# Kernel optimization log

Measured on AMD Instinct MI355X. Metric: run time of the kernel, lower is better.

The kernel has to match this reference:

```python
import jax, jax.numpy as jnp
import numpy as np

TEMP1, TEMP2, TEMP3 = 4.0, 5.0, 10.0
NORM_EPS = 1e-12   # F.normalize eps
COS_EPS = 1e-8     # custom_cosine_similarity eps


def setup_inputs() -> dict:
    key = jax.random.key(0)
    k1, k2 = jax.random.split(key)
    vis_embeds = jax.random.normal(k1, (16, 16, 16, 16, 128), dtype=jnp.float32)
    txt_embeds = jax.random.normal(k2, (16, 64, 128), dtype=jnp.float32)
    return {"vis_embeds": vis_embeds, "txt_embeds": txt_embeds}


def reference(vis_embeds, txt_embeds):
    # vis_embeds: [bs, h, w, d, E]; txt_embeds: [bs, T, E] (uniform token_len)
    bs, h, w, d, E = vis_embeds.shape
    S = h * w * d
    # L2-normalize along embedding dim (F.normalize)
    vn = vis_embeds / jnp.clip(jnp.linalg.norm(vis_embeds, axis=-1, keepdims=True), NORM_EPS)
    vn = vn.reshape(bs, S, E)                      # context, flattened source
    tn = txt_embeds / jnp.clip(jnp.linalg.norm(txt_embeds, axis=-1, keepdims=True), NORM_EPS)
    # attention_fn, vectorized over the outer loop index i (txt sample):
    # attn0[i,b,s,t] = <context_b[s], query_i[t]>
    attn0 = jnp.einsum('bse,ite->ibst', vn, tn)    # [bs_txt, bs_vis, S, T]
    s1 = jax.nn.softmax(attn0, axis=-1)            # softmax over query tokens t
    a = jax.nn.softmax(TEMP1 * jnp.swapaxes(s1, -1, -2), axis=-1)  # [i,b,t,s], softmax over s
    # weighted context: [i,b,t,E]
    wc = jnp.einsum('ibts,bse->ibte', a, vn)
    # custom cosine similarity along E between txt tokens and weighted context
    num = jnp.einsum('ibte,ite->ibt', wc, tn)
    w1 = jnp.linalg.norm(tn, axis=-1)              # [i,t] (== 1 up to normalize eps)
    w2 = jnp.linalg.norm(wc, axis=-1)              # [i,b,t]
    cos = num / jnp.clip(w1[:, None, :] * w2, COS_EPS)
    # row_sim: mul temp2, exp, sum over tokens (agg='sum'), log
    row = jnp.log(jnp.sum(jnp.exp(TEMP2 * cos), axis=-1))  # [i_txt, b_vis]
    sims = row.T * TEMP3                           # [b_vis, i_txt] matches torch cat(dim=1)
    labels = jnp.arange(bs)
    logp0 = jax.nn.log_softmax(sims, axis=-1)
    logp1 = jax.nn.log_softmax(sims.T, axis=-1)
    loss0 = -jnp.mean(logp0[labels, labels])
    loss1 = -jnp.mean(logp1[labels, labels])
    loss = (loss0 + loss1) / 2.0
    # att_maps: for sample i the original keeps attn[i] -> diagonal of [i,b,...]
    att_maps = a[labels, labels].reshape(bs, -1, h, w, d)  # [bs, T, h, w, d]
    return loss, att_maps
```

## Files before the change

kernel.cpp:

```cpp
#include <hip/hip_runtime.h>

constexpr int BS = 16;
constexpr int S  = 4096;
constexpr int E  = 128;
constexpr int T  = 64;
constexpr int NSP = 4;
constexpr int SSEG = S / NSP;
constexpr int CH = 128;
constexpr int NCH = SSEG / CH;
constexpr int ETS = 136;
constexpr int TNS = 136;
constexpr int PTS = 264;

constexpr long VN_OFF  = 0;
constexpr long VNT_OFF = (long)BS * S * E;
constexpr long WS_P    = (long)BS * S * E;
constexpr long WS_SIMS = WS_P + (long)256 * NSP * 8192;

typedef __attribute__((ext_vector_type(8))) short bf16x8;
typedef __attribute__((ext_vector_type(4))) float f32x4;

__device__ __forceinline__ unsigned short f2bf(float x) {
    unsigned u = __float_as_uint(x);
    u += 0x7FFFu + ((u >> 16) & 1u);
    return (unsigned short)(u >> 16);
}
__device__ __forceinline__ float bf2f(unsigned short v) {
    return __uint_as_float(((unsigned)v) << 16);
}

__global__ __launch_bounds__(512, 2)
void prep_kernel(const float* __restrict__ vis, unsigned short* __restrict__ wsv)
{
    __shared__ unsigned short Lt[128 * PTS];
    const int tid  = threadIdx.x;
    const int b    = blockIdx.x >> 5;
    const int tile = blockIdx.x & 31;
    const int s0   = tile * 128;
    const float* visb = vis + ((long)b * S + s0) * E;
    unsigned short* vn  = wsv + VN_OFF  + ((long)b * S + s0) * E;
    unsigned short* vnT = wsv + VNT_OFF + (long)b * E * S;

    {
        const int pp = tid >> 3, ee = tid & 7;
        const float* rA = visb + (long)(pp << 1) * E + (ee << 1);
        float2 va[8], vb[8];
        float sa = 0.f, sb = 0.f;
#pragma unroll
        for (int k = 0; k < 8; ++k) {
            va[k] = *(const float2*)(rA + (k << 4));
            vb[k] = *(const float2*)(rA + E + (k << 4));
            sa = fmaf(va[k].x, va[k].x, fmaf(va[k].y, va[k].y, sa));
            sb = fmaf(vb[k].x, vb[k].x, fmaf(vb[k].y, vb[k].y, sb));
        }
        sa += __shfl_xor(sa, 1); sa += __shfl_xor(sa, 2); sa += __shfl_xor(sa, 4);
        sb += __shfl_xor(sb, 1); sb += __shfl_xor(sb, 2); sb += __shfl_xor(sb, 4);
        const float ia = 1.0f / fmaxf(sqrtf(sa), 1e-12f);
        const float ib = 1.0f / fmaxf(sqrtf(sb), 1e-12f);
        const long r0 = (long)(pp << 1) * E, r1 = r0 + E;
#pragma unroll
        for (int k = 0; k < 8; ++k) {
            const int e0 = (ee << 1) + (k << 4);
            const unsigned ax = f2bf(va[k].x * ia), ay = f2bf(va[k].y * ia);
            const unsigned bx = f2bf(vb[k].x * ib), by = f2bf(vb[k].y * ib);
            *(unsigned*)&Lt[e0 * PTS + (pp << 1)]       = ax | (bx << 16);
            *(unsigned*)&Lt[(e0 + 1) * PTS + (pp << 1)] = ay | (by << 16);
            *(unsigned*)&vn[r0 + e0] = ax | (ay << 16);
            *(unsigned*)&vn[r1 + e0] = bx | (by << 16);
        }
    }
    __syncthreads();
    {
        const int e = tid >> 2, sseg = (tid & 3) << 5;
#pragma unroll
        for (int k = 0; k < 4; ++k) {
            const bf16x8 v = *(const bf16x8*)&Lt[e * PTS + sseg + (k << 3)];
            *(bf16x8*)&vnT[(long)e * S + s0 + sseg + (k << 3)] = v;
        }
    }
}

__global__ __launch_bounds__(512, 4)
void clip_main_kernel(const unsigned short* __restrict__ wsv,
                      const float* __restrict__ txt,
                      float* __restrict__ d_out,
                      float* __restrict__ wsf)
{
    __shared__ unsigned short ET[T * ETS];
    __shared__ unsigned short tnL[T * TNS];

    const int tid = threadIdx.x;
    const int w   = tid >> 6;
    const int l   = tid & 63;
    const int cl  = l & 15;
    const int q   = l >> 4;
    const int b   = blockIdx.x & 15;
    const int i   = (blockIdx.x >> 4) & 15;
    const int qt  = blockIdx.x >> 8;
    const bool diag = (i == b);

    {
        const int r = tid >> 3, seg = tid & 7;
        const float* tp = txt + ((long)i * T + r) * E + (seg << 4);
        const float4 a0 = *(const float4*)(tp);
        const float4 a1 = *(const float4*)(tp + 4);
        const float4 a2 = *(const float4*)(tp + 8);
        const float4 a3 = *(const float4*)(tp + 12);
        float ssq = a0.x*a0.x + a0.y*a0.y + a0.z*a0.z + a0.w*a0.w
                  + a1.x*a1.x + a1.y*a1.y + a1.z*a1.z + a1.w*a1.w
                  + a2.x*a2.x + a2.y*a2.y + a2.z*a2.z + a2.w*a2.w
                  + a3.x*a3.x + a3.y*a3.y + a3.z*a3.z + a3.w*a3.w;
        ssq += __shfl_xor(ssq, 1); ssq += __shfl_xor(ssq, 2); ssq += __shfl_xor(ssq, 4);
        const float inv = 1.0f / fmaxf(sqrtf(ssq), 1e-12f);
        bf16x8 f0, f1;
        f0[0]=(short)f2bf(a0.x*inv); f0[1]=(short)f2bf(a0.y*inv);
        f0[2]=(short)f2bf(a0.z*inv); f0[3]=(short)f2bf(a0.w*inv);
        f0[4]=(short)f2bf(a1.x*inv); f0[5]=(short)f2bf(a1.y*inv);
        f0[6]=(short)f2bf(a1.z*inv); f0[7]=(short)f2bf(a1.w*inv);
        f1[0]=(short)f2bf(a2.x*inv); f1[1]=(short)f2bf(a2.y*inv);
        f1[2]=(short)f2bf(a2.z*inv); f1[3]=(short)f2bf(a2.w*inv);
        f1[4]=(short)f2bf(a3.x*inv); f1[5]=(short)f2bf(a3.y*inv);
        f1[6]=(short)f2bf(a3.z*inv); f1[7]=(short)f2bf(a3.w*inv);
        *(bf16x8*)&tnL[r * TNS + (seg << 4)]     = f0;
        *(bf16x8*)&tnL[r * TNS + (seg << 4) + 8] = f1;
    }
    __syncthreads();

    f32x4 acc2[4];
#pragma unroll
    for (int n = 0; n < 4; ++n) acc2[n] = (f32x4){0.f,0.f,0.f,0.f};

    const unsigned short* vnb  = wsv + VN_OFF  + (long)b * S * E;
    const unsigned short* vntb = wsv + VNT_OFF + (long)b * E * S;
    float* attb = d_out + 1 + (long)b * (long)T * S;

    for (int ch = 0; ch < NCH; ++ch) {
        const int s0 = qt * SSEG + ch * CH;

        bf16x8 Bf[4];
        {
            const unsigned short* r0 = vnb + (long)(s0 + (w << 4) + cl) * E + (q << 3);
#pragma unroll
            for (int kk = 0; kk < 4; ++kk) Bf[kk] = *(const bf16x8*)(r0 + (kk << 5));
        }

        {
            f32x4 acc1[4];
#pragma unroll
            for (int mt = 0; mt < 4; ++mt) acc1[mt] = (f32x4){0.f,0.f,0.f,0.f};
#pragma unroll
            for (int kk = 0; kk < 4; ++kk)
#pragma unroll
                for (int mt = 0; mt < 4; ++mt) {
                    const bf16x8 tA = *(const bf16x8*)&tnL[((mt << 4) + cl) * TNS + (kk << 5) + (q << 3)];
                    acc1[mt] = __builtin_amdgcn_mfma_f32_16x16x32_bf16(tA, Bf[kk], acc1[mt], 0, 0, 0);
                }
            float ex[4][4];
            float ssum = 0.f;
#pragma unroll
            for (int mt = 0; mt < 4; ++mt)
#pragma unroll
                for (int r = 0; r < 4; ++r) {
                    const float v = __expf(acc1[mt][r]);
                    ex[mt][r] = v; ssum += v;
                }
            ssum += __shfl_xor(ssum, 16);
            ssum += __shfl_xor(ssum, 32);
            const float csc = 4.0f / ssum;
            const int sloc = (w << 4) + cl;
#pragma unroll
            for (int mt = 0; mt < 4; ++mt)
#pragma unroll
                for (int r = 0; r < 4; ++r)
                    ET[((mt << 4) + (q << 2) + r) * ETS + sloc] = f2bf(__expf(ex[mt][r] * csc));
        }
        __syncthreads();

        {
            const unsigned short* ar = vntb + (long)((w << 4) + cl) * S + s0 + (q << 3);
#pragma unroll
            for (int kk2 = 0; kk2 < 4; ++kk2) {
                const bf16x8 aV = *(const bf16x8*)(ar + (kk2 << 5));
#pragma unroll
                for (int n = 0; n < 4; ++n) {
                    const bf16x8 bE = *(const bf16x8*)&ET[((n << 4) + cl) * ETS + (kk2 << 5) + (q << 3)];
                    acc2[n] = __builtin_amdgcn_mfma_f32_16x16x32_bf16(aV, bE, acc2[n], 0, 0, 0);
                }
            }
        }

        if (diag) {
            const int t = tid >> 3, sg = (tid & 7) << 4;
            float* ap = attb + (long)t * S + s0 + sg;
            const bf16x8 v0 = *(const bf16x8*)&ET[t * ETS + sg];
            const bf16x8 v1 = *(const bf16x8*)&ET[t * ETS + sg + 8];
#pragma unroll
            for (int j = 0; j < 8; ++j) {
                ap[j]     = bf2f((unsigned short)v0[j]);
                ap[8 + j] = bf2f((unsigned short)v1[j]);
            }
        }
        __syncthreads();
    }

    {
        float* pp = wsf + WS_P + ((long)(((i << 4) + b) << 2) + qt) * 8192;
#pragma unroll
        for (int n = 0; n < 4; ++n)
#pragma unroll
            for (int r = 0; r < 4; ++r)
                pp[((w << 4) + (q << 2) + r) * 64 + (n << 4) + cl] = acc2[n][r];
    }
}

__global__ __launch_bounds__(256, 4)
void post_kernel(float* __restrict__ d_out, const float* __restrict__ txt,
                 float* __restrict__ wsf)
{
    const int tid = threadIdx.x;
    if (blockIdx.x >= BS * T) {
        __shared__ float sA[256], sB[256], sC[256];
        const int pair = blockIdx.x - BS * T;
        const int t = tid & 63, w4 = tid >> 6;
        const int i = pair >> 4, b = pair & 15;
        const float* p0 = wsf + WS_P + (long)pair * NSP * 8192;
        const float* tp = txt + ((long)i * T + t) * E + (w4 << 5);

        float ssq = 0.f, num = 0.f, w2 = 0.f;
#pragma unroll 8
        for (int e = 0; e < 32; ++e) {
            const float tv = tp[e];
            const int idx = ((w4 << 5) + e) * 64 + t;
            const float wc = p0[idx] + p0[idx + 8192] + p0[idx + 16384] + p0[idx + 24576];
            ssq = fmaf(tv, tv, ssq);
            num = fmaf(wc, tv, num);
            w2  = fmaf(wc, wc, w2);
        }
        sA[tid] = ssq; sB[tid] = num; sC[tid] = w2;
        __syncthreads();
        if (tid < 64) {
            const float ss = sA[tid] + sA[64 + tid] + sA[128 + tid] + sA[192 + tid];
            const float nm = sB[tid] + sB[64 + tid] + sB[128 + tid] + sB[192 + tid];
            const float ww = sC[tid] + sC[64 + tid] + sC[128 + tid] + sC[192 + tid];
            const float cosv = (nm / fmaxf(sqrtf(ss), 1e-12f)) / fmaxf(sqrtf(ww), 1e-20f);
            float r = __expf(5.0f * cosv);
#pragma unroll
            for (int m = 1; m < 64; m <<= 1) r += __shfl_xor(r, m);
            if (tid == 0) wsf[WS_SIMS + (b << 4) + i] = 10.0f * logf(r);
        }
        return;
    }
    __shared__ float r4[4];
    const int bt = blockIdx.x;
    float* p = d_out + 1 + (long)bt * 4096;
    float v[16];
    float s = 0.f;
#pragma unroll
    for (int k = 0; k < 16; ++k) { v[k] = p[k * 256 + tid]; s += v[k]; }
#pragma unroll
    for (int m = 1; m < 64; m <<= 1) s += __shfl_xor(s, m);
    if ((tid & 63) == 0) r4[tid >> 6] = s;
    __syncthreads();
    const float inv = 1.0f / (r4[0] + r4[1] + r4[2] + r4[3]);
#pragma unroll
    for (int k = 0; k < 16; ++k) p[k * 256 + tid] = v[k] * inv;
}

__global__ __launch_bounds__(256, 1)
void loss_kernel(const float* __restrict__ wsf, float* __restrict__ d_out)
{
    __shared__ float sm[16][17];
    __shared__ float red[16];
    const int tid = threadIdx.x;
    const int bb = tid >> 4, ii = tid & 15;
    const float x = wsf[WS_SIMS + bb * 16 + ii];
    sm[bb][ii] = x;
    float m = x;
#pragma unroll
    for (int msk = 1; msk < 16; msk <<= 1) m = fmaxf(m, __shfl_xor(m, msk));
    float s = __expf(x - m);
#pragma unroll
    for (int msk = 1; msk < 16; msk <<= 1) s += __shfl_xor(s, msk);
    const float lsm0 = x - m - logf(s);
    __syncthreads();
    const float y = sm[ii][bb];
    float m1 = y;
#pragma unroll
    for (int msk = 1; msk < 16; msk <<= 1) m1 = fmaxf(m1, __shfl_xor(m1, msk));
    float s1 = __expf(y - m1);
#pragma unroll
    for (int msk = 1; msk < 16; msk <<= 1) s1 += __shfl_xor(s1, msk);
    const float lsm1 = y - m1 - logf(s1);
    if (bb == ii) red[bb] = lsm0 + lsm1;
    __syncthreads();
    if (tid == 0) {
        float tot = 0.f;
#pragma unroll
        for (int k = 0; k < 16; ++k) tot += red[k];
        d_out[0] = -tot / 32.0f;
    }
}

extern "C" void kernel_launch(void* const* d_in, const int* in_sizes, int n_in,
                              void* d_out, int out_size, void* d_ws, size_t ws_size,
                              hipStream_t stream)
{
    const float* vis = (const float*)d_in[0];
    const float* txt = (const float*)d_in[1];
    float* out = (float*)d_out;
    unsigned short* wsv = (unsigned short*)d_ws;
    float* wsf = (float*)d_ws;

    hipLaunchKernelGGL(prep_kernel, dim3(512), dim3(512), 0, stream, vis, wsv);
    hipLaunchKernelGGL(clip_main_kernel, dim3(BS * BS * NSP), dim3(512), 0, stream,
                       wsv, txt, out, wsf);
    hipLaunchKernelGGL(post_kernel, dim3(BS * T + BS * BS), dim3(256), 0, stream,
                       out, txt, wsf);
    hipLaunchKernelGGL(loss_kernel, dim3(1), dim3(256), 0, stream, wsf, out);
}
```

Measured before the change: 192.4 us.

## Double-buffer exp tile in LDS, keep text fragments in registers, drop trailing barrier

The normalized text tile is read from LDS once into registers (16 bf16x8 fragments per lane) and reused for every chunk, instead of being reloaded from LDS each chunk. The exp-score tile ET is now double-buffered, which lets the second __syncthreads per chunk be removed. Global pointers are advanced incrementally. The cost is higher register pressure from the 64 extra VGPRs, which could reduce occupancy under the 512x4 launch bounds. The text staging buffer is reused as ET buffer 1. The first chunk iteration writes ET buffer 0 while other lanes may still be loading tnF from buffer 1, which is safe because those are different buffers. Buffer 1 is first written at ch=1, after a barrier.

```diff
diff --git a/kernel.cpp b/kernel.cpp
--- a/kernel.cpp
+++ b/kernel.cpp
@@ -9,7 +9,6 @@
 constexpr int CH = 128;
 constexpr int NCH = SSEG / CH;
 constexpr int ETS = 136;
-constexpr int TNS = 136;
 constexpr int PTS = 264;
 
 constexpr long VN_OFF  = 0;
@@ -86,8 +85,7 @@
                       float* __restrict__ d_out,
                       float* __restrict__ wsf)
 {
-    __shared__ unsigned short ET[T * ETS];
-    __shared__ unsigned short tnL[T * TNS];
+    __shared__ unsigned short ETb[2][T * ETS];
 
     const int tid = threadIdx.x;
     const int w   = tid >> 6;
@@ -121,10 +119,17 @@
         f1[2]=(short)f2bf(a2.z*inv); f1[3]=(short)f2bf(a2.w*inv);
         f1[4]=(short)f2bf(a3.x*inv); f1[5]=(short)f2bf(a3.y*inv);
         f1[6]=(short)f2bf(a3.z*inv); f1[7]=(short)f2bf(a3.w*inv);
-        *(bf16x8*)&tnL[r * TNS + (seg << 4)]     = f0;
-        *(bf16x8*)&tnL[r * TNS + (seg << 4) + 8] = f1;
-    }
-    __syncthreads();
+        *(bf16x8*)&ETb[1][r * ETS + (seg << 4)]     = f0;
+        *(bf16x8*)&ETb[1][r * ETS + (seg << 4) + 8] = f1;
+    }
+    __syncthreads();
+
+    bf16x8 tnF[4][4];
+#pragma unroll
+    for (int mt = 0; mt < 4; ++mt)
+#pragma unroll
+        for (int kk = 0; kk < 4; ++kk)
+            tnF[mt][kk] = *(const bf16x8*)&ETb[1][((mt << 4) + cl) * ETS + (kk << 5) + (q << 3)];
 
     f32x4 acc2[4];
 #pragma unroll
@@ -134,15 +139,15 @@
     const unsigned short* vntb = wsv + VNT_OFF + (long)b * E * S;
     float* attb = d_out + 1 + (long)b * (long)T * S;
 
+    const unsigned short* bfp = vnb  + (long)(qt * SSEG + (w << 4) + cl) * E + (q << 3);
+    const unsigned short* ar  = vntb + (long)((w << 4) + cl) * S + qt * SSEG + (q << 3);
+
     for (int ch = 0; ch < NCH; ++ch) {
-        const int s0 = qt * SSEG + ch * CH;
+        unsigned short* ET = ETb[ch & 1];
 
         bf16x8 Bf[4];
-        {
-            const unsigned short* r0 = vnb + (long)(s0 + (w << 4) + cl) * E + (q << 3);
-#pragma unroll
-            for (int kk = 0; kk < 4; ++kk) Bf[kk] = *(const bf16x8*)(r0 + (kk << 5));
-        }
+#pragma unroll
+        for (int kk = 0; kk < 4; ++kk) Bf[kk] = *(const bf16x8*)(bfp + (kk << 5));
 
         {
             f32x4 acc1[4];
@@ -151,18 +156,15 @@
 #pragma unroll
             for (int kk = 0; kk < 4; ++kk)
 #pragma unroll
-                for (int mt = 0; mt < 4; ++mt) {
-                    const bf16x8 tA = *(const bf16x8*)&tnL[((mt << 4) + cl) * TNS + (kk << 5) + (q << 3)];
-                    acc1[mt] = __builtin_amdgcn_mfma_f32_16x16x32_bf16(tA, Bf[kk], acc1[mt], 0, 0, 0);
-                }
-            float ex[4][4];
+                for (int mt = 0; mt < 4; ++mt)
+                    acc1[mt] = __builtin_amdgcn_mfma_f32_16x16x32_bf16(tnF[mt][kk], Bf[kk], acc1[mt], 0, 0, 0);
             float ssum = 0.f;
 #pragma unroll
             for (int mt = 0; mt < 4; ++mt)
 #pragma unroll
                 for (int r = 0; r < 4; ++r) {
                     const float v = __expf(acc1[mt][r]);
-                    ex[mt][r] = v; ssum += v;
+                    acc1[mt][r] = v; ssum += v;
                 }
             ssum += __shfl_xor(ssum, 16);
             ssum += __shfl_xor(ssum, 32);
@@ -172,24 +174,22 @@
             for (int mt = 0; mt < 4; ++mt)
 #pragma unroll
                 for (int r = 0; r < 4; ++r)
-                    ET[((mt << 4) + (q << 2) + r) * ETS + sloc] = f2bf(__expf(ex[mt][r] * csc));
+                    ET[((mt << 4) + (q << 2) + r) * ETS + sloc] = f2bf(__expf(acc1[mt][r] * csc));
         }
         __syncthreads();
 
-        {
-            const unsigned short* ar = vntb + (long)((w << 4) + cl) * S + s0 + (q << 3);
-#pragma unroll
-            for (int kk2 = 0; kk2 < 4; ++kk2) {
-                const bf16x8 aV = *(const bf16x8*)(ar + (kk2 << 5));
-#pragma unroll
-                for (int n = 0; n < 4; ++n) {
-                    const bf16x8 bE = *(const bf16x8*)&ET[((n << 4) + cl) * ETS + (kk2 << 5) + (q << 3)];
-                    acc2[n] = __builtin_amdgcn_mfma_f32_16x16x32_bf16(aV, bE, acc2[n], 0, 0, 0);
-                }
+#pragma unroll
+        for (int kk2 = 0; kk2 < 4; ++kk2) {
+            const bf16x8 aV = *(const bf16x8*)(ar + (kk2 << 5));
+#pragma unroll
+            for (int n = 0; n < 4; ++n) {
+                const bf16x8 bE = *(const bf16x8*)&ET[((n << 4) + cl) * ETS + (kk2 << 5) + (q << 3)];
+                acc2[n] = __builtin_amdgcn_mfma_f32_16x16x32_bf16(aV, bE, acc2[n], 0, 0, 0);
             }
         }
 
         if (diag) {
+            const int s0 = qt * SSEG + ch * CH;
             const int t = tid >> 3, sg = (tid & 7) << 4;
             float* ap = attb + (long)t * S + s0 + sg;
             const bf16x8 v0 = *(const bf16x8*)&ET[t * ETS + sg];
@@ -200,7 +200,9 @@
                 ap[8 + j] = bf2f((unsigned short)v1[j]);
             }
         }
-        __syncthreads();
+
+        bfp += CH * E;
+        ar  += CH;
     }
 
     {
```

New measurement: 204.0 us. 1.06x slower.

## Switch main kernel to 32x32x16 MFMA, larger S chunks, and precomputed text embeddings

Applied to the files above, without the earlier changes.

Moves text-embedding normalization out of the main kernel into a separate small kernel that writes bf16 normalized tokens to workspace. The main kernel then loads A fragments straight from global memory instead of staging them in LDS. It also doubles the S chunk to 256 and replaces the 16x16x32 MFMA tiling with 32x32x16 MFMAs, which halves the number of barriers per block and reduces LDS fragment reads. The cost is an extra kernel launch, higher register pressure from the 16-wide accumulators, and a larger ET LDS buffer that may lower occupancy.

```diff
diff --git a/kernel.cpp b/kernel.cpp
--- a/kernel.cpp
+++ b/kernel.cpp
@@ -6,19 +6,20 @@
 constexpr int T  = 64;
 constexpr int NSP = 4;
 constexpr int SSEG = S / NSP;
-constexpr int CH = 128;
+constexpr int CH = 256;
 constexpr int NCH = SSEG / CH;
-constexpr int ETS = 136;
-constexpr int TNS = 136;
+constexpr int ETS = 272;
 constexpr int PTS = 264;
 
 constexpr long VN_OFF  = 0;
 constexpr long VNT_OFF = (long)BS * S * E;
 constexpr long WS_P    = (long)BS * S * E;
 constexpr long WS_SIMS = WS_P + (long)256 * NSP * 8192;
+constexpr long TN_OFF  = (WS_SIMS + 256) * 2;
 
 typedef __attribute__((ext_vector_type(8))) short bf16x8;
 typedef __attribute__((ext_vector_type(4))) float f32x4;
+typedef __attribute__((ext_vector_type(16))) float f32x16;
 
 __device__ __forceinline__ unsigned short f2bf(float x) {
     unsigned u = __float_as_uint(x);
@@ -80,124 +81,124 @@
     }
 }
 
+__global__ __launch_bounds__(512, 2)
+void tn_prep_kernel(const float* __restrict__ txt, unsigned short* __restrict__ tnG)
+{
+    const int i = blockIdx.x, tid = threadIdx.x;
+    const int r = tid >> 3, seg = tid & 7;
+    const float* tp = txt + ((long)i * T + r) * E + (seg << 4);
+    const float4 a0 = *(const float4*)(tp);
+    const float4 a1 = *(const float4*)(tp + 4);
+    const float4 a2 = *(const float4*)(tp + 8);
+    const float4 a3 = *(const float4*)(tp + 12);
+    float ssq = a0.x*a0.x + a0.y*a0.y + a0.z*a0.z + a0.w*a0.w
+              + a1.x*a1.x + a1.y*a1.y + a1.z*a1.z + a1.w*a1.w
+              + a2.x*a2.x + a2.y*a2.y + a2.z*a2.z + a2.w*a2.w
+              + a3.x*a3.x + a3.y*a3.y + a3.z*a3.z + a3.w*a3.w;
+    ssq += __shfl_xor(ssq, 1); ssq += __shfl_xor(ssq, 2); ssq += __shfl_xor(ssq, 4);
+    const float inv = 1.0f / fmaxf(sqrtf(ssq), 1e-12f);
+    bf16x8 f0, f1;
+    f0[0]=(short)f2bf(a0.x*inv); f0[1]=(short)f2bf(a0.y*inv);
+    f0[2]=(short)f2bf(a0.z*inv); f0[3]=(short)f2bf(a0.w*inv);
+    f0[4]=(short)f2bf(a1.x*inv); f0[5]=(short)f2bf(a1.y*inv);
+    f0[6]=(short)f2bf(a1.z*inv); f0[7]=(short)f2bf(a1.w*inv);
+    f1[0]=(short)f2bf(a2.x*inv); f1[1]=(short)f2bf(a2.y*inv);
+    f1[2]=(short)f2bf(a2.z*inv); f1[3]=(short)f2bf(a2.w*inv);
+    f1[4]=(short)f2bf(a3.x*inv); f1[5]=(short)f2bf(a3.y*inv);
+    f1[6]=(short)f2bf(a3.z*inv); f1[7]=(short)f2bf(a3.w*inv);
+    unsigned short* o = tnG + ((long)i * T + r) * E + (seg << 4);
+    *(bf16x8*)o       = f0;
+    *(bf16x8*)(o + 8) = f1;
+}
+
 __global__ __launch_bounds__(512, 4)
 void clip_main_kernel(const unsigned short* __restrict__ wsv,
-                      const float* __restrict__ txt,
+                      const unsigned short* __restrict__ tnAll,
                       float* __restrict__ d_out,
                       float* __restrict__ wsf)
 {
     __shared__ unsigned short ET[T * ETS];
-    __shared__ unsigned short tnL[T * TNS];
 
     const int tid = threadIdx.x;
     const int w   = tid >> 6;
     const int l   = tid & 63;
-    const int cl  = l & 15;
-    const int q   = l >> 4;
+    const int lo  = l & 31;
+    const int hi  = l >> 5;
     const int b   = blockIdx.x & 15;
     const int i   = (blockIdx.x >> 4) & 15;
     const int qt  = blockIdx.x >> 8;
     const bool diag = (i == b);
 
-    {
-        const int r = tid >> 3, seg = tid & 7;
-        const float* tp = txt + ((long)i * T + r) * E + (seg << 4);
-        const float4 a0 = *(const float4*)(tp);
-        const float4 a1 = *(const float4*)(tp + 4);
-        const float4 a2 = *(const float4*)(tp + 8);
-        const float4 a3 = *(const float4*)(tp + 12);
-        float ssq = a0.x*a0.x + a0.y*a0.y + a0.z*a0.z + a0.w*a0.w
-                  + a1.x*a1.x + a1.y*a1.y + a1.z*a1.z + a1.w*a1.w
-                  + a2.x*a2.x + a2.y*a2.y + a2.z*a2.z + a2.w*a2.w
-                  + a3.x*a3.x + a3.y*a3.y + a3.z*a3.z + a3.w*a3.w;
-        ssq += __shfl_xor(ssq, 1); ssq += __shfl_xor(ssq, 2); ssq += __shfl_xor(ssq, 4);
-        const float inv = 1.0f / fmaxf(sqrtf(ssq), 1e-12f);
-        bf16x8 f0, f1;
-        f0[0]=(short)f2bf(a0.x*inv); f0[1]=(short)f2bf(a0.y*inv);
-        f0[2]=(short)f2bf(a0.z*inv); f0[3]=(short)f2bf(a0.w*inv);
-        f0[4]=(short)f2bf(a1.x*inv); f0[5]=(short)f2bf(a1.y*inv);
-        f0[6]=(short)f2bf(a1.z*inv); f0[7]=(short)f2bf(a1.w*inv);
-        f1[0]=(short)f2bf(a2.x*inv); f1[1]=(short)f2bf(a2.y*inv);
-        f1[2]=(short)f2bf(a2.z*inv); f1[3]=(short)f2bf(a2.w*inv);
-        f1[4]=(short)f2bf(a3.x*inv); f1[5]=(short)f2bf(a3.y*inv);
-        f1[6]=(short)f2bf(a3.z*inv); f1[7]=(short)f2bf(a3.w*inv);
-        *(bf16x8*)&tnL[r * TNS + (seg << 4)]     = f0;
-        *(bf16x8*)&tnL[r * TNS + (seg << 4) + 8] = f1;
-    }
-    __syncthreads();
-
-    f32x4 acc2[4];
-#pragma unroll
-    for (int n = 0; n < 4; ++n) acc2[n] = (f32x4){0.f,0.f,0.f,0.f};
-
+    const unsigned short* tnG  = tnAll + (long)i * T * E;
     const unsigned short* vnb  = wsv + VN_OFF  + (long)b * S * E;
     const unsigned short* vntb = wsv + VNT_OFF + (long)b * E * S;
     float* attb = d_out + 1 + (long)b * (long)T * S;
 
+    const unsigned short* pA0 = tnG + (long)lo * E + hi * 8;
+    const unsigned short* pA1 = tnG + (long)(32 + lo) * E + hi * 8;
+    const unsigned short* pB  = vnb + ((long)(qt * SSEG) + w * 32 + lo) * E + hi * 8;
+    const unsigned short* pV = vntb + ((long)((w >> 1) * 32 + lo)) * S + qt * SSEG + hi * 8;
+    const unsigned short* pE = &ET[((w & 1) * 32 + lo) * ETS + hi * 8];
+
+    f32x16 acc2;
+#pragma unroll
+    for (int r = 0; r < 16; ++r) acc2[r] = 0.f;
+
     for (int ch = 0; ch < NCH; ++ch) {
-        const int s0 = qt * SSEG + ch * CH;
-
-        bf16x8 Bf[4];
+        f32x16 a0, a1;
+#pragma unroll
+        for (int r = 0; r < 16; ++r) { a0[r] = 0.f; a1[r] = 0.f; }
         {
-            const unsigned short* r0 = vnb + (long)(s0 + (w << 4) + cl) * E + (q << 3);
-#pragma unroll
-            for (int kk = 0; kk < 4; ++kk) Bf[kk] = *(const bf16x8*)(r0 + (kk << 5));
+            const unsigned short* pBc = pB + (long)ch * CH * E;
+#pragma unroll
+            for (int kk = 0; kk < 8; ++kk) {
+                const bf16x8 Bf = *(const bf16x8*)(pBc + (kk << 4));
+                const bf16x8 A0 = *(const bf16x8*)(pA0 + (kk << 4));
+                const bf16x8 A1 = *(const bf16x8*)(pA1 + (kk << 4));
+                a0 = __builtin_amdgcn_mfma_f32_32x32x16_bf16(A0, Bf, a0, 0, 0, 0);
+                a1 = __builtin_amdgcn_mfma_f32_32x32x16_bf16(A1, Bf, a1, 0, 0, 0);
+            }
         }
 
         {
-            f32x4 acc1[4];
-#pragma unroll
-            for (int mt = 0; mt < 4; ++mt) acc1[mt] = (f32x4){0.f,0.f,0.f,0.f};
-#pragma unroll
-            for (int kk = 0; kk < 4; ++kk)
-#pragma unroll
-                for (int mt = 0; mt < 4; ++mt) {
-                    const bf16x8 tA = *(const bf16x8*)&tnL[((mt << 4) + cl) * TNS + (kk << 5) + (q << 3)];
-                    acc1[mt] = __builtin_amdgcn_mfma_f32_16x16x32_bf16(tA, Bf[kk], acc1[mt], 0, 0, 0);
-                }
-            float ex[4][4];
             float ssum = 0.f;
 #pragma unroll
-            for (int mt = 0; mt < 4; ++mt)
-#pragma unroll
-                for (int r = 0; r < 4; ++r) {
-                    const float v = __expf(acc1[mt][r]);
-                    ex[mt][r] = v; ssum += v;
-                }
-            ssum += __shfl_xor(ssum, 16);
+            for (int r = 0; r < 16; ++r) {
+                float v0 = __expf(a0[r]);
+                float v1 = __expf(a1[r]);
+                a0[r] = v0; a1[r] = v1;
+                ssum += v0 + v1;
+            }
             ssum += __shfl_xor(ssum, 32);
             const float csc = 4.0f / ssum;
-            const int sloc = (w << 4) + cl;
-#pragma unroll
-            for (int mt = 0; mt < 4; ++mt)
-#pragma unroll
-                for (int r = 0; r < 4; ++r)
-                    ET[((mt << 4) + (q << 2) + r) * ETS + sloc] = f2bf(__expf(ex[mt][r] * csc));
+            const int sl = (w << 5) + lo;
+#pragma unroll
+            for (int r = 0; r < 16; ++r) {
+                const int t0 = (r & 3) + ((r >> 2) << 3) + (hi << 2);
+                ET[t0 * ETS + sl]        = f2bf(__expf(a0[r] * csc));
+                ET[(32 + t0) * ETS + sl] = f2bf(__expf(a1[r] * csc));
+            }
         }
         __syncthreads();
 
         {
-            const unsigned short* ar = vntb + (long)((w << 4) + cl) * S + s0 + (q << 3);
-#pragma unroll
-            for (int kk2 = 0; kk2 < 4; ++kk2) {
-                const bf16x8 aV = *(const bf16x8*)(ar + (kk2 << 5));
-#pragma unroll
-                for (int n = 0; n < 4; ++n) {
-                    const bf16x8 bE = *(const bf16x8*)&ET[((n << 4) + cl) * ETS + (kk2 << 5) + (q << 3)];
-                    acc2[n] = __builtin_amdgcn_mfma_f32_16x16x32_bf16(aV, bE, acc2[n], 0, 0, 0);
-                }
+            const unsigned short* pVc = pV + ch * CH;
+#pragma unroll
+            for (int kk = 0; kk < 16; ++kk) {
+                const bf16x8 aF = *(const bf16x8*)(pVc + (kk << 4));
+                const bf16x8 bF = *(const bf16x8*)(pE + (kk << 4));
+                acc2 = __builtin_amdgcn_mfma_f32_32x32x16_bf16(aF, bF, acc2, 0, 0, 0);
             }
         }
 
         if (diag) {
-            const int t = tid >> 3, sg = (tid & 7) << 4;
-            float* ap = attb + (long)t * S + s0 + sg;
-            const bf16x8 v0 = *(const bf16x8*)&ET[t * ETS + sg];
-            const bf16x8 v1 = *(const bf16x8*)&ET[t * ETS + sg + 8];
-#pragma unroll
-            for (int j = 0; j < 8; ++j) {
-                ap[j]     = bf2f((unsigned short)v0[j]);
-                ap[8 + j] = bf2f((unsigned short)v1[j]);
+            const int t = tid >> 3, sg = (tid & 7) << 5;
+            float* ap = attb + (long)t * S + qt * SSEG + ch * CH + sg;
+#pragma unroll
+            for (int k2 = 0; k2 < 4; ++k2) {
+                const bf16x8 v = *(const bf16x8*)&ET[t * ETS + sg + (k2 << 3)];
+#pragma unroll
+                for (int j = 0; j < 8; ++j) ap[(k2 << 3) + j] = bf2f((unsigned short)v[j]);
             }
         }
         __syncthreads();
@@ -205,11 +206,13 @@
 
     {
         float* pp = wsf + WS_P + ((long)(((i << 4) + b) << 2) + qt) * 8192;
-#pragma unroll
-        for (int n = 0; n < 4; ++n)
-#pragma unroll
-            for (int r = 0; r < 4; ++r)
-                pp[((w << 4) + (q << 2) + r) * 64 + (n << 4) + cl] = acc2[n][r];
+        const int ebase = ((w >> 1) << 5) + (hi << 2);
+        const int tcol  = ((w & 1) << 5) + lo;
+#pragma unroll
+        for (int r = 0; r < 16; ++r) {
+            const int e = ebase + (r & 3) + ((r >> 2) << 3);
+            pp[e * 64 + tcol] = acc2[r];
+        }
     }
 }
 
@@ -312,8 +315,9 @@
     float* wsf = (float*)d_ws;
 
     hipLaunchKernelGGL(prep_kernel, dim3(512), dim3(512), 0, stream, vis, wsv);
+    hipLaunchKernelGGL(tn_prep_kernel, dim3(BS), dim3(512), 0, stream, txt, wsv + TN_OFF);
     hipLaunchKernelGGL(clip_main_kernel, dim3(BS * BS * NSP), dim3(512), 0, stream,
-                       wsv, txt, out, wsf);
+                       wsv, wsv + TN_OFF, out, wsf);
     hipLaunchKernelGGL(post_kernel, dim3(BS * T + BS * BS), dim3(256), 0, stream,
                        out, txt, wsf);
     hipLaunchKernelGGL(loss_kernel, dim3(1), dim3(256), 0, stream, wsf, out);
```

Measured after the change: 262.1 us. 1.36x slower.

## Use 32x32x16 MFMA for second GEMM and double-buffer ET to drop a barrier

Applied to the files above, without the earlier changes.

The second GEMM (weighted context) switches from four 16x16x32 MFMAs per k-step to a single 32x32x16 MFMA tile per wave, with a new fragment layout and a rewritten output scatter. The E-tile shared buffer is double-buffered by chunk parity, which removes the trailing __syncthreads per chunk iteration. Row pointers are hoisted out of the loop. This aims to cut LDS traffic per FLOP and one barrier per chunk, at the cost of more shared memory (which may affect occupancy) and correctness that depends on the 32x32 accumulator layout mapping.

```diff
diff --git a/kernel.cpp b/kernel.cpp
--- a/kernel.cpp
+++ b/kernel.cpp
@@ -19,6 +19,7 @@
 
 typedef __attribute__((ext_vector_type(8))) short bf16x8;
 typedef __attribute__((ext_vector_type(4))) float f32x4;
+typedef __attribute__((ext_vector_type(16))) float f32x16;
 
 __device__ __forceinline__ unsigned short f2bf(float x) {
     unsigned u = __float_as_uint(x);
@@ -86,7 +87,7 @@
                       float* __restrict__ d_out,
                       float* __restrict__ wsf)
 {
-    __shared__ unsigned short ET[T * ETS];
+    __shared__ unsigned short ETb[2][T * ETS];
     __shared__ unsigned short tnL[T * TNS];
 
     const int tid = threadIdx.x;
@@ -94,6 +95,8 @@
     const int l   = tid & 63;
     const int cl  = l & 15;
     const int q   = l >> 4;
+    const int lo  = l & 31;
+    const int hi  = l >> 5;
     const int b   = blockIdx.x & 15;
     const int i   = (blockIdx.x >> 4) & 15;
     const int qt  = blockIdx.x >> 8;
@@ -126,20 +129,24 @@
     }
     __syncthreads();
 
-    f32x4 acc2[4];
-#pragma unroll
-    for (int n = 0; n < 4; ++n) acc2[n] = (f32x4){0.f,0.f,0.f,0.f};
+    f32x16 acc2;
+#pragma unroll
+    for (int r = 0; r < 16; ++r) acc2[r] = 0.f;
 
     const unsigned short* vnb  = wsv + VN_OFF  + (long)b * S * E;
     const unsigned short* vntb = wsv + VNT_OFF + (long)b * E * S;
     float* attb = d_out + 1 + (long)b * (long)T * S;
 
+    const unsigned short* bfp = vnb  + (long)(qt * SSEG + (w << 4) + cl) * E + (q << 3);
+    const unsigned short* arp = vntb + (long)(((w >> 1) << 5) + lo) * S + qt * SSEG + (hi << 3);
+
     for (int ch = 0; ch < NCH; ++ch) {
+        unsigned short* ET = ETb[ch & 1];
         const int s0 = qt * SSEG + ch * CH;
 
         bf16x8 Bf[4];
         {
-            const unsigned short* r0 = vnb + (long)(s0 + (w << 4) + cl) * E + (q << 3);
+            const unsigned short* r0 = bfp + (long)ch * CH * E;
 #pragma unroll
             for (int kk = 0; kk < 4; ++kk) Bf[kk] = *(const bf16x8*)(r0 + (kk << 5));
         }
@@ -177,15 +184,13 @@
         __syncthreads();
 
         {
-            const unsigned short* ar = vntb + (long)((w << 4) + cl) * S + s0 + (q << 3);
-#pragma unroll
-            for (int kk2 = 0; kk2 < 4; ++kk2) {
-                const bf16x8 aV = *(const bf16x8*)(ar + (kk2 << 5));
-#pragma unroll
-                for (int n = 0; n < 4; ++n) {
-                    const bf16x8 bE = *(const bf16x8*)&ET[((n << 4) + cl) * ETS + (kk2 << 5) + (q << 3)];
-                    acc2[n] = __builtin_amdgcn_mfma_f32_16x16x32_bf16(aV, bE, acc2[n], 0, 0, 0);
-                }
+            const unsigned short* pVc = arp + ch * CH;
+            const unsigned short* pEb = &ET[(((w & 1) << 5) + lo) * ETS + (hi << 3)];
+#pragma unroll
+            for (int kk2 = 0; kk2 < 8; ++kk2) {
+                const bf16x8 aF = *(const bf16x8*)(pVc + (kk2 << 4));
+                const bf16x8 bF = *(const bf16x8*)(pEb + (kk2 << 4));
+                acc2 = __builtin_amdgcn_mfma_f32_32x32x16_bf16(aF, bF, acc2, 0, 0, 0);
             }
         }
 
@@ -200,16 +205,17 @@
                 ap[8 + j] = bf2f((unsigned short)v1[j]);
             }
         }
-        __syncthreads();
     }
 
     {
         float* pp = wsf + WS_P + ((long)(((i << 4) + b) << 2) + qt) * 8192;
-#pragma unroll
-        for (int n = 0; n < 4; ++n)
-#pragma unroll
-            for (int r = 0; r < 4; ++r)
-                pp[((w << 4) + (q << 2) + r) * 64 + (n << 4) + cl] = acc2[n][r];
+        const int ebase = ((w >> 1) << 5) + (hi << 2);
+        const int tcol  = ((w & 1) << 5) + lo;
+#pragma unroll
+        for (int r = 0; r < 16; ++r) {
+            const int e = ebase + (r & 3) + ((r >> 2) << 3);
+            pp[e * 64 + tcol] = acc2[r];
+        }
     }
 }
 
```

New measurement: 225.8 us. +17.3%, slower.
